# Performance work log

Hardware: AMD Instinct MI355X
Metric: run time of the kernel (lower is better)

Reference implementation:

```python
import jax, jax.numpy as jnp
import numpy as np

GROUPS = 8
EPS = 1e-3  # keras GroupNormalization default epsilon


def group_norm(x, gamma, beta):
    # x: [B,H,W,C], groups over channel axis
    B, H, W, C = x.shape
    g = GROUPS
    xr = x.reshape(B, H, W, g, C // g)
    mean = jnp.mean(xr, axis=(1, 2, 4), keepdims=True)
    var = jnp.var(xr, axis=(1, 2, 4), keepdims=True)
    xn = (xr - mean) * jax.lax.rsqrt(var + EPS)
    xn = xn.reshape(B, H, W, C)
    return xn * gamma + beta


def setup_inputs() -> dict:
    key = jax.random.key(0)
    ks = jax.random.split(key, 6)
    B, H, W, C = 8, 64, 64, 64
    std = 0.02
    return {
        "x": jax.random.normal(ks[0], (B, H, W, C), dtype=jnp.float32),
        "gamma": jnp.ones((C,), dtype=jnp.float32),
        "beta": jnp.zeros((C,), dtype=jnp.float32),
        "wq": jax.random.normal(ks[1], (C, C), dtype=jnp.float32) * std,
        "bq": jnp.zeros((C,), dtype=jnp.float32),
        "wk": jax.random.normal(ks[2], (C, C), dtype=jnp.float32) * std,
        "bk": jnp.zeros((C,), dtype=jnp.float32),
        "wv": jax.random.normal(ks[3], (C, C), dtype=jnp.float32) * std,
        "bv": jnp.zeros((C,), dtype=jnp.float32),
        "wp": jax.random.normal(ks[4], (C, C), dtype=jnp.float32) * std,
        "bp": jnp.zeros((C,), dtype=jnp.float32),
    }


def reference(x, gamma, beta, wq, bq, wk, bk, wv, bv, wp, bp):
    B, H, W, C = x.shape
    scale = jnp.asarray(C, x.dtype) ** -0.5
    h = group_norm(x, gamma, beta)  # note: residual uses normalized input (as in source)
    q = h @ wq + bq
    k = h @ wk + bk
    v = h @ wv + bv
    # full O((HW)^2) score tensor, exactly as the original
    attn = jnp.einsum('bhwc,bHWc->bhwHW', q, k) * scale
    attn = jax.nn.softmax(attn.reshape(B, H, W, H * W), axis=-1)
    attn = attn.reshape(B, H, W, H, W)
    proj = jnp.einsum('bhwHW,bHWc->bhwc', attn, v)
    proj = proj @ wp + bp
    return h + proj
```

## Files before the change

### kernel.cpp

```cpp
#include <hip/hip_runtime.h>

#define NTOK 4096
#define CH 64
#define LOG2E 1.4426950408889634f
#define QK_SCALE 0.42466090014400953f

typedef __bf16 bf8 __attribute__((ext_vector_type(8)));
typedef __bf16 bf4 __attribute__((ext_vector_type(4)));
typedef _Float16 h8 __attribute__((ext_vector_type(8)));
typedef _Float16 h4 __attribute__((ext_vector_type(4)));
typedef float f4 __attribute__((ext_vector_type(4)));
typedef long lx2 __attribute__((ext_vector_type(2)));

__device__ __forceinline__ f4 mfma16(bf8 a, bf8 b, f4 c) {
    return __builtin_amdgcn_mfma_f32_16x16x32_bf16(a, b, c, 0, 0, 0);
}
__device__ __forceinline__ f4 mfma8(long a, long b, f4 c) {
    return __builtin_amdgcn_mfma_f32_16x16x32_fp8_fp8(a, b, c, 0, 0, 0);
}
__device__ __forceinline__ unsigned char to_fp8(float v) {
    return (unsigned char)(__builtin_amdgcn_cvt_pk_fp8_f32(v, v, 0, false) & 0xff);
}

__global__ __launch_bounds__(256) void pre_kernel(const float* __restrict__ wq,
                                                  const float* __restrict__ wk,
                                                  const float* __restrict__ wv,
                                                  const float* __restrict__ wp,
                                                  const float* __restrict__ x,
                                                  __bf16* __restrict__ wqt,
                                                  __bf16* __restrict__ wkt,
                                                  __bf16* __restrict__ wvt,
                                                  __bf16* __restrict__ wpt,
                                                  float* __restrict__ gpart) {
    int t = threadIdx.x;
    if (blockIdx.x < 4) {
        int m = blockIdx.x;
        const float* src = (m == 0) ? wq : (m == 1) ? wk : (m == 2) ? wv : wp;
        __bf16* dst      = (m == 0) ? wqt : (m == 1) ? wkt : (m == 2) ? wvt : wpt;
        __shared__ float s[64][65];
        for (int i = 0; i < 16; ++i) {
            int e = i * 256 + t;
            s[e >> 6][e & 63] = src[e];
        }
        __syncthreads();
        int o = t >> 2, seg = t & 3;
        for (int j = 0; j < 16; ++j) {
            int in = seg * 16 + j;
            dst[o * 64 + in] = (__bf16)s[in][o];
        }
        return;
    }
    int bid = blockIdx.x - 4;
    int b = bid >> 6, slab = bid & 63;
    const float4* xb = (const float4*)(x + (size_t)(b * NTOK + slab * 64) * CH);
    float s = 0.f, ss = 0.f;
    for (int i = 0; i < 4; ++i) {
        int row = (t >> 4) + i * 16;
        float4 v = xb[row * 16 + (t & 15)];
        s  += v.x + v.y + v.z + v.w;
        ss += v.x * v.x + v.y * v.y + v.z * v.z + v.w * v.w;
    }
    __shared__ float ls[256], lss[256];
    ls[t] = s; lss[t] = ss;
    __syncthreads();
    if (t < 8) {
        float a = 0.f, aa = 0.f;
        for (int p = 0; p < 16; ++p) {
            a  += ls[p * 16 + 2 * t]  + ls[p * 16 + 2 * t + 1];
            aa += lss[p * 16 + 2 * t] + lss[p * 16 + 2 * t + 1];
        }
        gpart[((b * 64 + slab) * 8 + t) * 2 + 0] = a;
        gpart[((b * 64 + slab) * 8 + t) * 2 + 1] = aa;
    }
}

__global__ __launch_bounds__(256) void qkv_gn(const float* __restrict__ x,
                                              const float* __restrict__ gpart,
                                              const float* __restrict__ gamma,
                                              const float* __restrict__ beta,
                                              const __bf16* __restrict__ wqt,
                                              const __bf16* __restrict__ wkt,
                                              const __bf16* __restrict__ wvt,
                                              const float* __restrict__ bq,
                                              const float* __restrict__ bk,
                                              const float* __restrict__ bv,
                                              unsigned char* __restrict__ qp,
                                              unsigned char* __restrict__ kp,
                                              unsigned char* __restrict__ vp) {
    __shared__ __bf16 W[3][64][72];
    __shared__ _Float16 Vst[64][68];
    __shared__ unsigned char Qst[64][72];
    __shared__ unsigned char Kst[64][72];
    __shared__ float red[128];
    __shared__ float sstat[16];
    __shared__ float sg[64], sb2[64];
    int t = threadIdx.x;
    size_t rowbase = (size_t)blockIdx.x * 64;
    int b = (int)(rowbase >> 12), tokbase = (int)(rowbase & 4095);
    int lane = t & 63, wave = t >> 6, quad = lane >> 4, l15 = lane & 15;
    int row = wave * 16 + l15;

    const float* xr = x + (rowbase + row) * 64;
    float4 xl0 = *(const float4*)(xr + quad * 8);
    float4 xl1 = *(const float4*)(xr + quad * 8 + 4);
    float4 xh0 = *(const float4*)(xr + 32 + quad * 8);
    float4 xh1 = *(const float4*)(xr + 32 + quad * 8 + 4);

    for (int m = 0; m < 3; ++m) {
        const __bf16* src = (m == 0) ? wqt : (m == 1) ? wkt : wvt;
        for (int i = 0; i < 2; ++i) {
            int e = i * 256 + t, rr = e >> 3, ch = e & 7;
            *(bf8*)&W[m][rr][ch * 8] = *(const bf8*)(src + rr * 64 + ch * 8);
        }
    }
    if (t < 64) { sg[t] = gamma[t]; sb2[t] = beta[t]; }
    if (t < 64) {
        int gi = t & 7, c = t >> 3;
        const float2* gp = (const float2*)gpart + (size_t)b * 512 + gi;
        float a = 0.f, aa = 0.f;
        for (int p = c * 8; p < c * 8 + 8; ++p) {
            float2 v = gp[(size_t)p * 8];
            a += v.x; aa += v.y;
        }
        red[t * 2] = a; red[t * 2 + 1] = aa;
    }
    __syncthreads();
    if (t < 8) {
        float a = 0.f, aa = 0.f;
        for (int c = 0; c < 8; ++c) {
            a  += red[(c * 8 + t) * 2];
            aa += red[(c * 8 + t) * 2 + 1];
        }
        float mean = a * (1.f / 32768.f);
        float var = aa * (1.f / 32768.f) - mean * mean;
        sstat[t * 2 + 0] = mean;
        sstat[t * 2 + 1] = rsqrtf(var + 1e-3f);
    }
    __syncthreads();

    bf8 a0, a1;
    {
        float mlo = sstat[quad * 2], rlo = sstat[quad * 2 + 1];
        float mhi = sstat[(4 + quad) * 2], rhi = sstat[(4 + quad) * 2 + 1];
        float xl[8] = {xl0.x, xl0.y, xl0.z, xl0.w, xl1.x, xl1.y, xl1.z, xl1.w};
        float xh[8] = {xh0.x, xh0.y, xh0.z, xh0.w, xh1.x, xh1.y, xh1.z, xh1.w};
#pragma unroll
        for (int j = 0; j < 8; ++j) {
            int c = quad * 8 + j;
            a0[j] = (__bf16)((xl[j] - mlo) * sg[c] * rlo + sb2[c]);
            a1[j] = (__bf16)((xh[j] - mhi) * sg[32 + c] * rhi + sb2[32 + c]);
        }
    }

    for (int m = 0; m < 3; ++m) {
        const float* bias = (m == 0) ? bq : (m == 1) ? bk : bv;
        float sc = (m == 2) ? 1.0f : QK_SCALE;
        for (int tt = 0; tt < 4; ++tt) {
            int col = l15 + 16 * tt;
            bf8 b0 = *(const bf8*)&W[m][col][quad * 8];
            bf8 b1 = *(const bf8*)&W[m][col][32 + quad * 8];
            f4 acc = {0.f, 0.f, 0.f, 0.f};
            acc = mfma16(a0, b0, acc);
            acc = mfma16(a1, b1, acc);
            float bb = bias[col];
            if (m == 2) {
                for (int r = 0; r < 4; ++r)
                    Vst[col][wave * 16 + quad * 4 + r] = (_Float16)(acc[r] + bb);
            } else if (m == 1) {
                for (int r = 0; r < 4; ++r)
                    Kst[wave * 16 + quad * 4 + r][col] = to_fp8((acc[r] + bb) * sc);
            } else {
                for (int r = 0; r < 4; ++r)
                    Qst[wave * 16 + quad * 4 + r][col] = to_fp8((acc[r] + bb) * sc);
            }
        }
    }
    __syncthreads();
    {
        const unsigned char* krow = &Kst[wave * 16 + l15][0];
        lx2 kk; kk[0] = *(const long*)(krow + quad * 8);
        kk[1] = *(const long*)(krow + 32 + quad * 8);
        *(lx2*)(kp + (((size_t)b * 256 + (tokbase >> 4) + wave) * 64 + lane) * 16) = kk;
        const unsigned char* qrow = &Qst[wave * 16 + l15][0];
        lx2 qq; qq[0] = *(const long*)(qrow + quad * 8);
        qq[1] = *(const long*)(qrow + 32 + quad * 8);
        *(lx2*)(qp + (((size_t)b * 256 + (tokbase >> 4) + wave) * 64 + lane) * 16) = qq;
    }
    {
        int d = wave * 16 + l15;
        for (int kb = 0; kb < 2; ++kb) {
            h4 lo = *(const h4*)&Vst[d][kb * 32 + quad * 4];
            h4 hi = *(const h4*)&Vst[d][kb * 32 + 16 + quad * 4];
            int d0 = __builtin_amdgcn_cvt_pk_fp8_f32((float)lo[0], (float)lo[1], 0, false);
            d0     = __builtin_amdgcn_cvt_pk_fp8_f32((float)lo[2], (float)lo[3], d0, true);
            int d1 = __builtin_amdgcn_cvt_pk_fp8_f32((float)hi[0], (float)hi[1], 0, false);
            d1     = __builtin_amdgcn_cvt_pk_fp8_f32((float)hi[2], (float)hi[3], d1, true);
            long v8 = (long)(unsigned int)d0 | ((long)d1 << 32);
            int kt = (tokbase >> 5) + kb;
            *(long*)(vp + ((((size_t)b * 128 + kt) * 2 + (wave >> 1)) * 64 + lane) * 16
                        + (wave & 1) * 8) = v8;
        }
    }
}

__device__ __forceinline__ void load_kv(const unsigned char* kpw, const unsigned char* vpw,
                                        long kf[4], long vf[4]) {
    lx2 a = *(const lx2*)(kpw);
    lx2 b = *(const lx2*)(kpw + 1024);
    lx2 c = *(const lx2*)(vpw);
    lx2 d = *(const lx2*)(vpw + 1024);
    kf[0] = a[0]; kf[1] = a[1]; kf[2] = b[0]; kf[3] = b[1];
    vf[0] = c[0]; vf[1] = c[1]; vf[2] = d[0]; vf[3] = d[1];
}

__device__ __forceinline__ void compute32(const long kf[4], const long vf[4],
                                          const long aqlo[4], const long aqhi[4],
                                          long ones, f4 acc[4][4], f4 acc_li[4]) {
#pragma unroll
    for (int s = 0; s < 4; ++s) {
        f4 St0 = {0.f, 0.f, 0.f, 0.f};
        f4 St1 = {0.f, 0.f, 0.f, 0.f};
        St0 = mfma8(kf[0], aqlo[s], St0);
        St0 = mfma8(kf[1], aqhi[s], St0);
        St1 = mfma8(kf[2], aqlo[s], St1);
        St1 = mfma8(kf[3], aqhi[s], St1);
        float p00 = __builtin_amdgcn_exp2f(St0[0]);
        float p01 = __builtin_amdgcn_exp2f(St0[1]);
        float p02 = __builtin_amdgcn_exp2f(St0[2]);
        float p03 = __builtin_amdgcn_exp2f(St0[3]);
        float p10 = __builtin_amdgcn_exp2f(St1[0]);
        float p11 = __builtin_amdgcn_exp2f(St1[1]);
        float p12 = __builtin_amdgcn_exp2f(St1[2]);
        float p13 = __builtin_amdgcn_exp2f(St1[3]);
        int d0 = __builtin_amdgcn_cvt_pk_fp8_f32(p00, p01, 0, false);
        d0     = __builtin_amdgcn_cvt_pk_fp8_f32(p02, p03, d0, true);
        int d1 = __builtin_amdgcn_cvt_pk_fp8_f32(p10, p11, 0, false);
        d1     = __builtin_amdgcn_cvt_pk_fp8_f32(p12, p13, d1, true);
        long pf = (long)(unsigned int)d0 | ((long)d1 << 32);
        acc_li[s] = mfma8(ones, pf, acc_li[s]);
        acc[s][0] = mfma8(vf[0], pf, acc[s][0]);
        acc[s][1] = mfma8(vf[1], pf, acc[s][1]);
        acc[s][2] = mfma8(vf[2], pf, acc[s][2]);
        acc[s][3] = mfma8(vf[3], pf, acc[s][3]);
    }
}

__global__ __launch_bounds__(256, 2) void attn_final(const unsigned char* __restrict__ qp,
                                                     const unsigned char* __restrict__ kp,
                                                     const unsigned char* __restrict__ vp,
                                                     const __bf16* __restrict__ wpt,
                                                     const float* __restrict__ bp,
                                                     const float* __restrict__ x,
                                                     const float* __restrict__ gpart,
                                                     const float* __restrict__ gamma,
                                                     const float* __restrict__ beta,
                                                     float* __restrict__ out) {
    __shared__ _Float16 Om[2][64][72];
    __shared__ float sS[2][64];
    __shared__ __bf16 Wl[64][72];
    __shared__ __bf16 Ol[64][72];
    __shared__ float red[128];
    __shared__ float sstat[16], sg[64], sb[64];

    int bid = blockIdx.x;
    int qt = bid >> 3, b = bid & 7;
    int t = threadIdx.x, lane = t & 63, w = t >> 6, quad = lane >> 4, l15 = lane & 15;

    for (int i = 0; i < 2; ++i) {
        int e = i * 256 + t, row = e >> 3, ch = e & 7;
        *(bf8*)&Wl[row][ch * 8] = *(const bf8*)(wpt + row * 64 + ch * 8);
    }
    if (t < 64) { sg[t] = gamma[t]; sb[t] = beta[t]; }
    if (t < 64) {
        int gi = t & 7, c = t >> 3;
        const float2* gp = (const float2*)gpart + (size_t)b * 512 + gi;
        float a = 0.f, aa = 0.f;
        for (int p = c * 8; p < c * 8 + 8; ++p) {
            float2 v = gp[(size_t)p * 8];
            a += v.x; aa += v.y;
        }
        red[t * 2] = a; red[t * 2 + 1] = aa;
    }

    const unsigned char* qpb = qp + (((size_t)b * 256 + qt * 4) * 64 + lane) * 16;
    long aqlo[4], aqhi[4];
    for (int s = 0; s < 4; ++s) {
        lx2 qq = *(const lx2*)(qpb + (size_t)s * 1024);
        aqlo[s] = qq[0]; aqhi[s] = qq[1];
    }
    const unsigned char* kpw = kp + ((size_t)b * 256 + w * 64) * 1024 + lane * 16;
    const unsigned char* vpw = vp + ((size_t)b * 128 + w * 32) * 2048 + lane * 16;

    const long ones = 0x3838383838383838L;

    f4 acc[4][4] = {};
    f4 acc_li[4] = {};

    long kfA[4], kfB[4], vfA[4], vfB[4];
    load_kv(kpw, vpw, kfA, vfA);
    for (int it = 0; it < 32; it += 2) {
        load_kv(kpw + (size_t)(it + 1) * 2048, vpw + (size_t)(it + 1) * 2048, kfB, vfB);
        __builtin_amdgcn_s_setprio(1);
        compute32(kfA, vfA, aqlo, aqhi, ones, acc, acc_li);
        __builtin_amdgcn_s_setprio(0);
        if (it + 2 < 32)
            load_kv(kpw + (size_t)(it + 2) * 2048, vpw + (size_t)(it + 2) * 2048, kfA, vfA);
        __builtin_amdgcn_s_setprio(1);
        compute32(kfB, vfB, aqlo, aqhi, ones, acc, acc_li);
        __builtin_amdgcn_s_setprio(0);
    }

    float li[4];
#pragma unroll
    for (int s = 0; s < 4; ++s) li[s] = acc_li[s][0];

    if (w >= 2) {
        for (int s = 0; s < 4; ++s) {
            for (int td = 0; td < 4; ++td) {
                h4 o4;
                for (int r = 0; r < 4; ++r) o4[r] = (_Float16)acc[s][td][r];
                *(h4*)&Om[w - 2][s * 16 + l15][td * 16 + quad * 4] = o4;
            }
            if (quad == 0) sS[w - 2][s * 16 + l15] = li[s];
        }
    }
    __syncthreads();
    if (t < 8) {
        float a = 0.f, aa = 0.f;
        for (int c = 0; c < 8; ++c) {
            a  += red[(c * 8 + t) * 2];
            aa += red[(c * 8 + t) * 2 + 1];
        }
        float mean = a * (1.f / 32768.f);
        float var = aa * (1.f / 32768.f) - mean * mean;
        sstat[t * 2 + 0] = mean;
        sstat[t * 2 + 1] = rsqrtf(var + 1e-3f);
    }
    if (w < 2) {
        for (int s = 0; s < 4; ++s) {
            for (int td = 0; td < 4; ++td) {
                h4 o4 = *(const h4*)&Om[w][s * 16 + l15][td * 16 + quad * 4];
                for (int r = 0; r < 4; ++r) acc[s][td][r] += (float)o4[r];
            }
            li[s] += sS[w][s * 16 + l15];
        }
    }
    __syncthreads();
    if (w < 2) {
        for (int s = 0; s < 4; ++s) {
            for (int td = 0; td < 4; ++td) {
                h4 o4;
                for (int r = 0; r < 4; ++r) o4[r] = (_Float16)acc[s][td][r];
                *(h4*)&Om[w][s * 16 + l15][td * 16 + quad * 4] = o4;
            }
            if (quad == 0) sS[w][s * 16 + l15] = li[s];
        }
    }
    __syncthreads();
    {
        int qq = t >> 2, ds = (t & 3) * 16;
        float inv = 1.f / (sS[0][qq] + sS[1][qq]);
        h8 a0 = *(const h8*)&Om[0][qq][ds];
        h8 b0 = *(const h8*)&Om[0][qq][ds + 8];
        h8 a1 = *(const h8*)&Om[1][qq][ds];
        h8 b1 = *(const h8*)&Om[1][qq][ds + 8];
        bf8 olo, ohi;
        for (int j = 0; j < 8; ++j) {
            olo[j] = (__bf16)(((float)a0[j] + (float)a1[j]) * inv);
            ohi[j] = (__bf16)(((float)b0[j] + (float)b1[j]) * inv);
        }
        *(bf8*)&Ol[qq][ds] = olo;
        *(bf8*)&Ol[qq][ds + 8] = ohi;
    }
    __syncthreads();
    size_t rowbase = ((size_t)b * NTOK + qt * 64) + w * 16;
    bf8 a0 = *(const bf8*)&Ol[w * 16 + l15][quad * 8];
    bf8 a1 = *(const bf8*)&Ol[w * 16 + l15][32 + quad * 8];
    for (int tt = 0; tt < 4; ++tt) {
        int col = l15 + 16 * tt;
        bf8 b0 = *(const bf8*)&Wl[col][quad * 8];
        bf8 b1 = *(const bf8*)&Wl[col][32 + quad * 8];
        f4 pacc = {0.f, 0.f, 0.f, 0.f};
        pacc = mfma16(a0, b0, pacc);
        pacc = mfma16(a1, b1, pacc);
        int grp = col >> 3;
        float mean = sstat[grp * 2], gs = sg[col] * sstat[grp * 2 + 1], bs = sb[col];
        float bias = bp[col];
        for (int r = 0; r < 4; ++r) {
            size_t gi = (rowbase + quad * 4 + r) * 64 + col;
            float h = (x[gi] - mean) * gs + bs;
            out[gi] = pacc[r] + bias + h;
        }
    }
}

extern "C" void kernel_launch(void* const* d_in, const int* in_sizes, int n_in,
                              void* d_out, int out_size, void* d_ws, size_t ws_size,
                              hipStream_t stream) {
    const float* x     = (const float*)d_in[0];
    const float* gamma = (const float*)d_in[1];
    const float* beta  = (const float*)d_in[2];
    const float* wq    = (const float*)d_in[3];
    const float* bq    = (const float*)d_in[4];
    const float* wk    = (const float*)d_in[5];
    const float* bk    = (const float*)d_in[6];
    const float* wv    = (const float*)d_in[7];
    const float* bv    = (const float*)d_in[8];
    const float* wp    = (const float*)d_in[9];
    const float* bp    = (const float*)d_in[10];
    float* out = (float*)d_out;

    char* ws = (char*)d_ws;
    const size_t MB = 1024 * 1024;
    unsigned char* qpb = (unsigned char*)(ws);
    unsigned char* kpb = (unsigned char*)(ws + 2 * MB);
    unsigned char* vpb = (unsigned char*)(ws + 4 * MB);
    __bf16*   wqt  = (__bf16*)(ws + 12 * MB);
    __bf16*   wkt  = (__bf16*)(ws + 12 * MB + 8192);
    __bf16*   wvt  = (__bf16*)(ws + 12 * MB + 16384);
    __bf16*   wpt  = (__bf16*)(ws + 12 * MB + 24576);
    float*    gpart = (float*)(ws + 12 * MB + 32768);

    pre_kernel<<<516, 256, 0, stream>>>(wq, wk, wv, wp, x, wqt, wkt, wvt, wpt, gpart);
    qkv_gn<<<512, 256, 0, stream>>>(x, gpart, gamma, beta, wqt, wkt, wvt, bq, bk, bv,
                                    qpb, kpb, vpb);
    attn_final<<<512, 256, 0, stream>>>(qpb, kpb, vpb, wpt, bp, x, gpart, gamma, beta, out);
}
```

Baseline: 118.6 us.

## Split attention key range across eight waves per block instead of four

After: 124.4 us. +4.9%, slower.

```diff
diff --git a/kernel.cpp b/kernel.cpp
--- a/kernel.cpp
+++ b/kernel.cpp
@@ -245,7 +245,7 @@
     }
 }
 
-__global__ __launch_bounds__(256, 2) void attn_final(const unsigned char* __restrict__ qp,
+__global__ __launch_bounds__(512, 2) void attn_final(const unsigned char* __restrict__ qp,
                                                      const unsigned char* __restrict__ kp,
                                                      const unsigned char* __restrict__ vp,
                                                      const __bf16* __restrict__ wpt,
@@ -255,8 +255,8 @@
                                                      const float* __restrict__ gamma,
                                                      const float* __restrict__ beta,
                                                      float* __restrict__ out) {
-    __shared__ _Float16 Om[2][64][72];
-    __shared__ float sS[2][64];
+    __shared__ _Float16 Om[4][64][72];
+    __shared__ float sS[4][64];
     __shared__ __bf16 Wl[64][72];
     __shared__ __bf16 Ol[64][72];
     __shared__ float red[128];
@@ -266,11 +266,11 @@
     int qt = bid >> 3, b = bid & 7;
     int t = threadIdx.x, lane = t & 63, w = t >> 6, quad = lane >> 4, l15 = lane & 15;
 
-    for (int i = 0; i < 2; ++i) {
-        int e = i * 256 + t, row = e >> 3, ch = e & 7;
+    {
+        int row = t >> 3, ch = t & 7;
         *(bf8*)&Wl[row][ch * 8] = *(const bf8*)(wpt + row * 64 + ch * 8);
     }
-    if (t < 64) { sg[t] = gamma[t]; sb[t] = beta[t]; }
+    if (t >= 64 && t < 128) { int u = t - 64; sg[u] = gamma[u]; sb[u] = beta[u]; }
     if (t < 64) {
         int gi = t & 7, c = t >> 3;
         const float2* gp = (const float2*)gpart + (size_t)b * 512 + gi;
@@ -284,29 +284,24 @@
 
     const unsigned char* qpb = qp + (((size_t)b * 256 + qt * 4) * 64 + lane) * 16;
     long aqlo[4], aqhi[4];
+#pragma unroll
     for (int s = 0; s < 4; ++s) {
         lx2 qq = *(const lx2*)(qpb + (size_t)s * 1024);
         aqlo[s] = qq[0]; aqhi[s] = qq[1];
     }
-    const unsigned char* kpw = kp + ((size_t)b * 256 + w * 64) * 1024 + lane * 16;
-    const unsigned char* vpw = vp + ((size_t)b * 128 + w * 32) * 2048 + lane * 16;
+    const unsigned char* kpw = kp + ((size_t)b * 256 + w * 32) * 1024 + lane * 16;
+    const unsigned char* vpw = vp + ((size_t)b * 128 + w * 16) * 2048 + lane * 16;
 
     const long ones = 0x3838383838383838L;
 
     f4 acc[4][4] = {};
     f4 acc_li[4] = {};
 
-    long kfA[4], kfB[4], vfA[4], vfB[4];
-    load_kv(kpw, vpw, kfA, vfA);
-    for (int it = 0; it < 32; it += 2) {
-        load_kv(kpw + (size_t)(it + 1) * 2048, vpw + (size_t)(it + 1) * 2048, kfB, vfB);
+    long kf[4], vf[4];
+    for (int it = 0; it < 16; ++it) {
+        load_kv(kpw + (size_t)it * 2048, vpw + (size_t)it * 2048, kf, vf);
         __builtin_amdgcn_s_setprio(1);
-        compute32(kfA, vfA, aqlo, aqhi, ones, acc, acc_li);
-        __builtin_amdgcn_s_setprio(0);
-        if (it + 2 < 32)
-            load_kv(kpw + (size_t)(it + 2) * 2048, vpw + (size_t)(it + 2) * 2048, kfA, vfA);
-        __builtin_amdgcn_s_setprio(1);
-        compute32(kfB, vfB, aqlo, aqhi, ones, acc, acc_li);
+        compute32(kf, vf, aqlo, aqhi, ones, acc, acc_li);
         __builtin_amdgcn_s_setprio(0);
     }
 
@@ -314,7 +309,39 @@
 #pragma unroll
     for (int s = 0; s < 4; ++s) li[s] = acc_li[s][0];
 
-    if (w >= 2) {
+    if (w >= 4) {
+        for (int s = 0; s < 4; ++s) {
+            for (int td = 0; td < 4; ++td) {
+                h4 o4;
+                for (int r = 0; r < 4; ++r) o4[r] = (_Float16)acc[s][td][r];
+                *(h4*)&Om[w - 4][s * 16 + l15][td * 16 + quad * 4] = o4;
+            }
+            if (quad == 0) sS[w - 4][s * 16 + l15] = li[s];
+        }
+    }
+    __syncthreads();
+    if (t < 8) {
+        float a = 0.f, aa = 0.f;
+        for (int c = 0; c < 8; ++c) {
+            a  += red[(c * 8 + t) * 2];
+            aa += red[(c * 8 + t) * 2 + 1];
+        }
+        float mean = a * (1.f / 32768.f);
+        float var = aa * (1.f / 32768.f) - mean * mean;
+        sstat[t * 2 + 0] = mean;
+        sstat[t * 2 + 1] = rsqrtf(var + 1e-3f);
+    }
+    if (w < 4) {
+        for (int s = 0; s < 4; ++s) {
+            for (int td = 0; td < 4; ++td) {
+                h4 o4 = *(const h4*)&Om[w][s * 16 + l15][td * 16 + quad * 4];
+                for (int r = 0; r < 4; ++r) acc[s][td][r] += (float)o4[r];
+            }
+            li[s] += sS[w][s * 16 + l15];
+        }
+    }
+    __syncthreads();
+    if (w >= 2 && w < 4) {
         for (int s = 0; s < 4; ++s) {
             for (int td = 0; td < 4; ++td) {
                 h4 o4;
@@ -325,17 +352,6 @@
         }
     }
     __syncthreads();
-    if (t < 8) {
-        float a = 0.f, aa = 0.f;
-        for (int c = 0; c < 8; ++c) {
-            a  += red[(c * 8 + t) * 2];
-            aa += red[(c * 8 + t) * 2 + 1];
-        }
-        float mean = a * (1.f / 32768.f);
-        float var = aa * (1.f / 32768.f) - mean * mean;
-        sstat[t * 2 + 0] = mean;
-        sstat[t * 2 + 1] = rsqrtf(var + 1e-3f);
-    }
     if (w < 2) {
         for (int s = 0; s < 4; ++s) {
             for (int td = 0; td < 4; ++td) {
@@ -358,38 +374,37 @@
     }
     __syncthreads();
     {
-        int qq = t >> 2, ds = (t & 3) * 16;
+        int qq = t >> 3, ds = (t & 7) * 8;
         float inv = 1.f / (sS[0][qq] + sS[1][qq]);
         h8 a0 = *(const h8*)&Om[0][qq][ds];
-        h8 b0 = *(const h8*)&Om[0][qq][ds + 8];
         h8 a1 = *(const h8*)&Om[1][qq][ds];
-        h8 b1 = *(const h8*)&Om[1][qq][ds + 8];
-        bf8 olo, ohi;
-        for (int j = 0; j < 8; ++j) {
-            olo[j] = (__bf16)(((float)a0[j] + (float)a1[j]) * inv);
-            ohi[j] = (__bf16)(((float)b0[j] + (float)b1[j]) * inv);
-        }
-        *(bf8*)&Ol[qq][ds] = olo;
-        *(bf8*)&Ol[qq][ds + 8] = ohi;
-    }
-    __syncthreads();
-    size_t rowbase = ((size_t)b * NTOK + qt * 64) + w * 16;
-    bf8 a0 = *(const bf8*)&Ol[w * 16 + l15][quad * 8];
-    bf8 a1 = *(const bf8*)&Ol[w * 16 + l15][32 + quad * 8];
-    for (int tt = 0; tt < 4; ++tt) {
-        int col = l15 + 16 * tt;
-        bf8 b0 = *(const bf8*)&Wl[col][quad * 8];
-        bf8 b1 = *(const bf8*)&Wl[col][32 + quad * 8];
-        f4 pacc = {0.f, 0.f, 0.f, 0.f};
-        pacc = mfma16(a0, b0, pacc);
-        pacc = mfma16(a1, b1, pacc);
-        int grp = col >> 3;
-        float mean = sstat[grp * 2], gs = sg[col] * sstat[grp * 2 + 1], bs = sb[col];
-        float bias = bp[col];
-        for (int r = 0; r < 4; ++r) {
-            size_t gi = (rowbase + quad * 4 + r) * 64 + col;
-            float h = (x[gi] - mean) * gs + bs;
-            out[gi] = pacc[r] + bias + h;
+        bf8 o;
+        for (int j = 0; j < 8; ++j)
+            o[j] = (__bf16)(((float)a0[j] + (float)a1[j]) * inv);
+        *(bf8*)&Ol[qq][ds] = o;
+    }
+    __syncthreads();
+    {
+        int wr = w & 3, wh = w >> 2;
+        size_t rowbase = ((size_t)b * NTOK + qt * 64) + wr * 16;
+        bf8 a0 = *(const bf8*)&Ol[wr * 16 + l15][quad * 8];
+        bf8 a1 = *(const bf8*)&Ol[wr * 16 + l15][32 + quad * 8];
+        for (int tth = 0; tth < 2; ++tth) {
+            int tt = wh * 2 + tth;
+            int col = l15 + 16 * tt;
+            bf8 b0 = *(const bf8*)&Wl[col][quad * 8];
+            bf8 b1 = *(const bf8*)&Wl[col][32 + quad * 8];
+            f4 pacc = {0.f, 0.f, 0.f, 0.f};
+            pacc = mfma16(a0, b0, pacc);
+            pacc = mfma16(a1, b1, pacc);
+            int grp = col >> 3;
+            float mean = sstat[grp * 2], gs = sg[col] * sstat[grp * 2 + 1], bs = sb[col];
+            float bias = bp[col];
+            for (int r = 0; r < 4; ++r) {
+                size_t gi = (rowbase + quad * 4 + r) * 64 + col;
+                float h = (x[gi] - mean) * gs + bs;
+                out[gi] = pacc[r] + bias + h;
+            }
         }
     }
 }
@@ -424,5 +439,5 @@
     pre_kernel<<<516, 256, 0, stream>>>(wq, wk, wv, wp, x, wqt, wkt, wvt, wpt, gpart);
     qkv_gn<<<512, 256, 0, stream>>>(x, gpart, gamma, beta, wqt, wkt, wvt, bq, bk, bv,
                                     qpb, kpb, vpb);
-    attn_final<<<512, 256, 0, stream>>>(qpb, kpb, vpb, wpt, bp, x, gpart, gamma, beta, out);
-}
+    attn_final<<<512, 512, 0, stream>>>(qpb, kpb, vpb, wpt, bp, x, gpart, gamma, beta, out);
+}
```
